# Kernel optimization log

Hardware: AMD Instinct MI355X
Metric: run time of the kernel (lower is better)

The kernel has to match this reference:

```python
import jax, jax.numpy as jnp
import numpy as np

EPS = 1e-8  # torch.nn.CosineSimilarity default eps
N, D = 8192, 256


def setup_inputs() -> dict:
    key = jax.random.key(0)
    kq, kr = jax.random.split(key)
    query = jax.random.normal(kq, (N, D), dtype=jnp.float32)
    response = jax.random.normal(kr, (N, D), dtype=jnp.float32)
    return {"query": query, "response": response}


def reference(query, response):
    # cosine sim via one GEMM on raw vectors, normalized by clamped norm product
    # torch: x.y / max(||x||*||y||, eps)
    qn = jnp.linalg.norm(query, axis=-1)          # [N]
    rn = jnp.linalg.norm(response, axis=-1)       # [N]
    dots = query @ response.T                     # [N, N]
    denom = jnp.maximum(qn[:, None] * rn[None, :], EPS)
    all_score = dots / denom                      # [N, N] cosine sims
    pos_score = jnp.diagonal(all_score)           # [N]
    lse = jax.nn.logsumexp(all_score, axis=-1)    # [N]
    loss = jnp.sum(pos_score - lse)
    return -loss
```

## Files before the change

### kernel.cpp

```cpp
#include <hip/hip_runtime.h>
#include <hip/hip_bf16.h>

#define DDIM   256
#define BROWS  256
#define BN      64
#define NT       8
#define TS   (BN * DDIM)
#define SQRT_LOG2E 1.2011224087864498f

typedef float f32x4 __attribute__((ext_vector_type(4)));
typedef int   i32x4 __attribute__((ext_vector_type(4)));
typedef int   i32x8 __attribute__((ext_vector_type(8)));

__device__ __forceinline__ float exp2_hw(float x) {
  return __builtin_amdgcn_exp2f(x);
}

__device__ __forceinline__ f32x4 mfma_mx(i32x8 a, i32x8 b, f32x4 c) {
  return __builtin_amdgcn_mfma_scale_f32_16x16x128_f8f6f4(
      a, b, c, 0, 0, 0, 0x7F7F7F7F, 0, 0x7F7F7F7F);
}

__device__ __forceinline__ i32x8 cat8(i32x4 lo, i32x4 hi) {
  return __builtin_shufflevector(lo, hi, 0, 1, 2, 3, 4, 5, 6, 7);
}

__device__ __forceinline__ unsigned int pack4_fp8(float a0, float a1, float a2, float a3) {
  int v = __builtin_amdgcn_cvt_pk_fp8_f32(a0, a1, 0, false);
  v = __builtin_amdgcn_cvt_pk_fp8_f32(a2, a3, v, true);
  return (unsigned int)v;
}

__global__ __launch_bounds__(256) void prep_kernel(
    const float* __restrict__ q, const float* __restrict__ r,
    unsigned char* __restrict__ qf8, unsigned char* __restrict__ rf8,
    float* __restrict__ pos, float* __restrict__ row_sum) {
  int lane = threadIdx.x & 63, wave = threadIdx.x >> 6;
  int row = blockIdx.x * 4 + wave;
  size_t base = (size_t)row * DDIM + lane * 4;
  float4 qv = *(const float4*)(q + base);
  float4 rv = *(const float4*)(r + base);
  float qq = qv.x*qv.x + qv.y*qv.y + qv.z*qv.z + qv.w*qv.w;
  float rr = rv.x*rv.x + rv.y*rv.y + rv.z*rv.z + rv.w*rv.w;
  float qr = qv.x*rv.x + qv.y*rv.y + qv.z*rv.z + qv.w*rv.w;
  #pragma unroll
  for (int m = 1; m < 64; m <<= 1) {
    qq += __shfl_xor(qq, m);
    rr += __shfl_xor(rr, m);
    qr += __shfl_xor(qr, m);
  }
  float iq0 = 1.0f / sqrtf(qq);
  float ir0 = 1.0f / sqrtf(rr);
  float iq = iq0 * SQRT_LOG2E;
  float ir = ir0 * SQRT_LOG2E;
  unsigned int qp = pack4_fp8(qv.x*iq, qv.y*iq, qv.z*iq, qv.w*iq);
  unsigned int rp = pack4_fp8(rv.x*ir, rv.y*ir, rv.z*ir, rv.w*ir);
  *(unsigned int*)(qf8 + base) = qp;
  *(unsigned int*)(rf8 + base) = rp;
  if (lane == 0) {
    pos[row] = qr * iq0 * ir0;
    row_sum[row] = 0.0f;
  }
}

__device__ __forceinline__ void stage_quarter(char* dstBase,
                                              const unsigned char* src_base,
                                              int col0, int q, int tid) {
  int ch = q * 256 + tid;
  int c   = ch & 15;
  int g   = (ch >> 4) & 3;
  int pc  = (ch >> 6) & 1;
  int h   = (ch >> 7) & 1;
  int cf  = (ch >> 8) & 1;
  int p   = (ch >> 9) & 1;
  int col = p * 32 + cf * 16 + c;
  int src = col * 256 + h * 128 + g * 32 + pc * 16;
  __builtin_amdgcn_global_load_lds(
      (const __attribute__((address_space(1))) void*)((const char*)src_base + (size_t)col0 * 256 + src),
      (__attribute__((address_space(3))) void*)(dstBase + ch * 16),
      16, 0, 0);
}

__global__ __launch_bounds__(256, 2) void gemm_lse_kernel(
    const unsigned char* __restrict__ qf8, const unsigned char* __restrict__ rf8,
    float* __restrict__ row_sum) {
  __shared__ __attribute__((aligned(16))) unsigned char Bl[3 * TS];

  const int tid  = threadIdx.x;
  const int lane = tid & 63;
  const int wid  = tid >> 6;
  const int g = lane >> 4, c = lane & 15;
  const int row0  = blockIdx.x * BROWS;
  const int col00 = blockIdx.y * (NT * BN);
  const unsigned char* Rb = rf8;

  #pragma unroll
  for (int q = 0; q < 4; ++q) stage_quarter((char*)Bl,      Rb, col00,      q, tid);
  #pragma unroll
  for (int q = 0; q < 4; ++q) stage_quarter((char*)Bl + TS, Rb, col00 + BN, q, tid);

  i32x8 av[4][2];
  const char* Ab = (const char*)qf8;
  #pragma unroll
  for (int m = 0; m < 4; ++m) {
    size_t rb0 = (size_t)(row0 + wid * 64 + m * 16 + c) * 256;
    #pragma unroll
    for (int h = 0; h < 2; ++h) {
      const char* p = Ab + rb0 + h * 128 + g * 32;
      av[m][h] = cat8(*(const i32x4*)(p), *(const i32x4*)(p + 16));
    }
  }

  float rs[16];
  #pragma unroll
  for (int k = 0; k < 16; ++k) rs[k] = 0.0f;

  asm volatile("s_waitcnt vmcnt(4)" ::: "memory");
  __builtin_amdgcn_s_barrier();

  int rb = 0;
  int wb = 2 * TS;
  for (int t = 0; t < NT; ++t) {
    const char* lbase = (const char*)Bl + rb + lane * 16;
    #pragma unroll
    for (int p = 0; p < 2; ++p) {
      if (t + 2 < NT) {
        stage_quarter((char*)Bl + wb, Rb, col00 + (t + 2) * BN, 2 * p,     tid);
        stage_quarter((char*)Bl + wb, Rb, col00 + (t + 2) * BN, 2 * p + 1, tid);
      }

      i32x8 bv[2][2];
      #pragma unroll
      for (int cf = 0; cf < 2; ++cf)
        #pragma unroll
        for (int h = 0; h < 2; ++h) {
          const int off = (p * 8 + cf * 4 + h * 2) * 1024;
          bv[cf][h] = cat8(*(const i32x4*)(lbase + off),
                           *(const i32x4*)(lbase + off + 1024));
        }

      f32x4 acc[4][2];
      const f32x4 zero = {0.f, 0.f, 0.f, 0.f};
      #pragma unroll
      for (int m = 0; m < 4; ++m) { acc[m][0] = zero; acc[m][1] = zero; }
      __builtin_amdgcn_s_setprio(1);
      #pragma unroll
      for (int m = 0; m < 4; ++m)
        #pragma unroll
        for (int cf = 0; cf < 2; ++cf) {
          acc[m][cf] = mfma_mx(av[m][0], bv[cf][0], acc[m][cf]);
          acc[m][cf] = mfma_mx(av[m][1], bv[cf][1], acc[m][cf]);
        }
      __builtin_amdgcn_s_setprio(0);

      #pragma unroll
      for (int m = 0; m < 4; ++m)
        #pragma unroll
        for (int jj = 0; jj < 4; ++jj)
          rs[m * 4 + jj] += exp2_hw(acc[m][0][jj]);
      #pragma unroll
      for (int m = 0; m < 4; ++m)
        #pragma unroll
        for (int jj = 0; jj < 4; ++jj)
          rs[m * 4 + jj] += exp2_hw(acc[m][1][jj]);
    }

    if (t + 2 < NT) asm volatile("s_waitcnt vmcnt(4)" ::: "memory");
    else            asm volatile("s_waitcnt vmcnt(0)" ::: "memory");
    __builtin_amdgcn_s_barrier();

    rb += TS; if (rb == 3 * TS) rb = 0;
    wb += TS; if (wb == 3 * TS) wb = 0;
  }

  #pragma unroll
  for (int k = 0; k < 16; ++k) {
    float v = rs[k];
    v += __shfl_xor(v, 1);
    v += __shfl_xor(v, 2);
    v += __shfl_xor(v, 4);
    v += __shfl_xor(v, 8);
    if (c == 0) {
      int row = row0 + wid * 64 + (k >> 2) * 16 + g * 4 + (k & 3);
      atomicAdd(&row_sum[row], v);
    }
  }
}

__global__ __launch_bounds__(1024) void finalize_kernel(
    const float* __restrict__ row_sum, const float* __restrict__ pos,
    float* __restrict__ out, int n) {
  int t = threadIdx.x;
  float s = 0.f;
  #pragma unroll 4
  for (int i = t; i < n; i += 1024) s += __logf(row_sum[i]) - pos[i];
  #pragma unroll
  for (int m = 1; m < 64; m <<= 1) s += __shfl_xor(s, m);
  __shared__ float red[16];
  if ((t & 63) == 0) red[t >> 6] = s;
  __syncthreads();
  if (t == 0) {
    float tot = 0.f;
    #pragma unroll
    for (int w = 0; w < 16; ++w) tot += red[w];
    out[0] = tot;
  }
}

extern "C" void kernel_launch(void* const* d_in, const int* in_sizes, int n_in,
                              void* d_out, int out_size, void* d_ws, size_t ws_size,
                              hipStream_t stream) {
  const float* q = (const float*)d_in[0];
  const float* r = (const float*)d_in[1];
  int n = in_sizes[0] / DDIM;

  char* w = (char*)d_ws;
  size_t f8Bytes = (size_t)n * DDIM;
  unsigned char* qf8 = (unsigned char*)w;
  unsigned char* rf8 = (unsigned char*)(w + f8Bytes);
  float* pos     = (float*)(w + 2 * f8Bytes);
  float* row_sum = pos + n;

  prep_kernel<<<n / 4, 256, 0, stream>>>(q, r, qf8, rf8, pos, row_sum);

  dim3 grid(n / BROWS, n / (NT * BN));
  gemm_lse_kernel<<<grid, 256, 0, stream>>>(qf8, rf8, row_sum);

  finalize_kernel<<<1, 1024, 0, stream>>>(row_sum, pos, (float*)d_out, n);
}
```

Baseline: 34.36 us.

## Halve column tiles per block, double-buffer B, parallelize finalize with atomics

Each GEMM block now covers 4 column tiles instead of 8, which doubles the grid. The triple-buffered B pipeline (prefetch distance 2, 48KB LDS) becomes a double buffer (prefetch distance 1, 32KB LDS), so LDS use drops and occupancy may rise. The single-block finalize is replaced by a multi-block reduction that atomically accumulates into an output zeroed in the prep kernel. The costs are shorter per-block amortization of the A-register loads and a shallower prefetch that may expose load latency, plus more atomics on row_sum and on the output.

```diff
diff --git a/kernel.cpp b/kernel.cpp
--- a/kernel.cpp
+++ b/kernel.cpp
@@ -4,7 +4,7 @@
 #define DDIM   256
 #define BROWS  256
 #define BN      64
-#define NT       8
+#define NT       4
 #define TS   (BN * DDIM)
 #define SQRT_LOG2E 1.2011224087864498f
 
@@ -34,7 +34,9 @@
 __global__ __launch_bounds__(256) void prep_kernel(
     const float* __restrict__ q, const float* __restrict__ r,
     unsigned char* __restrict__ qf8, unsigned char* __restrict__ rf8,
-    float* __restrict__ pos, float* __restrict__ row_sum) {
+    float* __restrict__ pos, float* __restrict__ row_sum,
+    float* __restrict__ out) {
+  if (blockIdx.x == 0 && threadIdx.x == 0) out[0] = 0.0f;
   int lane = threadIdx.x & 63, wave = threadIdx.x >> 6;
   int row = blockIdx.x * 4 + wave;
   size_t base = (size_t)row * DDIM + lane * 4;
@@ -84,7 +86,7 @@
 __global__ __launch_bounds__(256, 2) void gemm_lse_kernel(
     const unsigned char* __restrict__ qf8, const unsigned char* __restrict__ rf8,
     float* __restrict__ row_sum) {
-  __shared__ __attribute__((aligned(16))) unsigned char Bl[3 * TS];
+  __shared__ __attribute__((aligned(16))) unsigned char Bl[2 * TS];
 
   const int tid  = threadIdx.x;
   const int lane = tid & 63;
@@ -95,9 +97,7 @@
   const unsigned char* Rb = rf8;
 
   #pragma unroll
-  for (int q = 0; q < 4; ++q) stage_quarter((char*)Bl,      Rb, col00,      q, tid);
-  #pragma unroll
-  for (int q = 0; q < 4; ++q) stage_quarter((char*)Bl + TS, Rb, col00 + BN, q, tid);
+  for (int q = 0; q < 4; ++q) stage_quarter((char*)Bl, Rb, col00, q, tid);
 
   i32x8 av[4][2];
   const char* Ab = (const char*)qf8;
@@ -115,20 +115,21 @@
   #pragma unroll
   for (int k = 0; k < 16; ++k) rs[k] = 0.0f;
 
-  asm volatile("s_waitcnt vmcnt(4)" ::: "memory");
+  asm volatile("s_waitcnt vmcnt(0)" ::: "memory");
   __builtin_amdgcn_s_barrier();
 
   int rb = 0;
-  int wb = 2 * TS;
   for (int t = 0; t < NT; ++t) {
+    if (t + 1 < NT) {
+      char* wbuf = (char*)Bl + (rb ^ TS);
+      #pragma unroll
+      for (int q = 0; q < 4; ++q)
+        stage_quarter(wbuf, Rb, col00 + (t + 1) * BN, q, tid);
+    }
+
     const char* lbase = (const char*)Bl + rb + lane * 16;
     #pragma unroll
     for (int p = 0; p < 2; ++p) {
-      if (t + 2 < NT) {
-        stage_quarter((char*)Bl + wb, Rb, col00 + (t + 2) * BN, 2 * p,     tid);
-        stage_quarter((char*)Bl + wb, Rb, col00 + (t + 2) * BN, 2 * p + 1, tid);
-      }
-
       i32x8 bv[2][2];
       #pragma unroll
       for (int cf = 0; cf < 2; ++cf)
@@ -165,12 +166,9 @@
           rs[m * 4 + jj] += exp2_hw(acc[m][1][jj]);
     }
 
-    if (t + 2 < NT) asm volatile("s_waitcnt vmcnt(4)" ::: "memory");
-    else            asm volatile("s_waitcnt vmcnt(0)" ::: "memory");
+    asm volatile("s_waitcnt vmcnt(0)" ::: "memory");
     __builtin_amdgcn_s_barrier();
-
-    rb += TS; if (rb == 3 * TS) rb = 0;
-    wb += TS; if (wb == 3 * TS) wb = 0;
+    rb ^= TS;
   }
 
   #pragma unroll
@@ -187,24 +185,18 @@
   }
 }
 
-__global__ __launch_bounds__(1024) void finalize_kernel(
+__global__ __launch_bounds__(256) void finalize_kernel(
     const float* __restrict__ row_sum, const float* __restrict__ pos,
-    float* __restrict__ out, int n) {
-  int t = threadIdx.x;
-  float s = 0.f;
-  #pragma unroll 4
-  for (int i = t; i < n; i += 1024) s += __logf(row_sum[i]) - pos[i];
+    float* __restrict__ out) {
+  int i = blockIdx.x * 256 + threadIdx.x;
+  float s = __logf(row_sum[i]) - pos[i];
   #pragma unroll
   for (int m = 1; m < 64; m <<= 1) s += __shfl_xor(s, m);
-  __shared__ float red[16];
-  if ((t & 63) == 0) red[t >> 6] = s;
+  __shared__ float red[4];
+  if ((threadIdx.x & 63) == 0) red[threadIdx.x >> 6] = s;
   __syncthreads();
-  if (t == 0) {
-    float tot = 0.f;
-    #pragma unroll
-    for (int w = 0; w < 16; ++w) tot += red[w];
-    out[0] = tot;
-  }
+  if (threadIdx.x == 0)
+    atomicAdd(out, red[0] + red[1] + red[2] + red[3]);
 }
 
 extern "C" void kernel_launch(void* const* d_in, const int* in_sizes, int n_in,
@@ -221,10 +213,11 @@
   float* pos     = (float*)(w + 2 * f8Bytes);
   float* row_sum = pos + n;
 
-  prep_kernel<<<n / 4, 256, 0, stream>>>(q, r, qf8, rf8, pos, row_sum);
+  prep_kernel<<<n / 4, 256, 0, stream>>>(q, r, qf8, rf8, pos, row_sum,
+                                         (float*)d_out);
 
   dim3 grid(n / BROWS, n / (NT * BN));
   gemm_lse_kernel<<<grid, 256, 0, stream>>>(qf8, rf8, row_sum);
 
-  finalize_kernel<<<1, 1024, 0, stream>>>(row_sum, pos, (float*)d_out, n);
-}
+  finalize_kernel<<<n / 256, 256, 0, stream>>>(row_sum, pos, (float*)d_out);
+}
```

Result: slower. 134.7 us (+291.9%).
